# Performance work log

Measured on AMD Instinct MI355X. Metric: run time of the kernel, lower is better.

The kernel has to match this reference:

```python
import jax, jax.numpy as jnp
import numpy as np

B, V, H_DIM, W_DIM = 4, 4, 256, 384
D_SH = 1  # sh_degree=0, pred_color=False -> (0+1)^2
SCALE_MIN, SCALE_MAX = 1e-05, 30.0
EPS = 1e-08


def _quat_to_mat(q):  # (...,4) wxyz unit quat -> (...,3,3)
    w, x, y, z = q[..., 0], q[..., 1], q[..., 2], q[..., 3]
    return jnp.stack([
        jnp.stack([1 - 2 * (y * y + z * z), 2 * (x * y - w * z), 2 * (x * z + w * y)], -1),
        jnp.stack([2 * (x * y + w * z), 1 - 2 * (x * x + z * z), 2 * (y * z - w * x)], -1),
        jnp.stack([2 * (x * z - w * y), 2 * (y * z + w * x), 1 - 2 * (x * x + y * y)], -1),
    ], -2)


def _mat_to_quat_wxyz(m):  # (...,3,3) rotation -> (...,4) wxyz
    m00, m01, m02 = m[..., 0, 0], m[..., 0, 1], m[..., 0, 2]
    m10, m11, m12 = m[..., 1, 0], m[..., 1, 1], m[..., 1, 2]
    m20, m21, m22 = m[..., 2, 0], m[..., 2, 1], m[..., 2, 2]
    q_abs = jnp.sqrt(jnp.maximum(0.0, jnp.stack([
        1.0 + m00 + m11 + m22, 1.0 + m00 - m11 - m22,
        1.0 - m00 + m11 - m22, 1.0 - m00 - m11 + m22], -1)))
    cand = jnp.stack([
        jnp.stack([q_abs[..., 0] ** 2, m21 - m12, m02 - m20, m10 - m01], -1),
        jnp.stack([m21 - m12, q_abs[..., 1] ** 2, m10 + m01, m02 + m20], -1),
        jnp.stack([m02 - m20, m10 + m01, q_abs[..., 2] ** 2, m12 + m21], -1),
        jnp.stack([m10 - m01, m20 + m02, m21 + m12, q_abs[..., 3] ** 2], -1),
    ], -2)
    cand = cand / (2.0 * jnp.maximum(q_abs[..., None], 0.1))
    idx = jnp.argmax(q_abs, axis=-1)
    q = jnp.take_along_axis(cand, idx[..., None, None], axis=-2)[..., 0, :]
    return q / jnp.linalg.norm(q, axis=-1, keepdims=True)


def _quat_mul_wxyz(a, b):
    aw, ax, ay, az = a[..., 0], a[..., 1], a[..., 2], a[..., 3]
    bw, bx, by, bz = b[..., 0], b[..., 1], b[..., 2], b[..., 3]
    return jnp.stack([
        aw * bw - ax * bx - ay * by - az * bz,
        aw * bx + ax * bw + ay * bz - az * by,
        aw * by - ax * bz + ay * bw + az * bx,
        aw * bz + ax * by - ay * bx + az * bw], -1)


def setup_inputs() -> dict:
    key = jax.random.key(0)
    k1, k2, k3, k4, k5, k6 = jax.random.split(key, 6)
    # valid world->cam extrinsics: rotation from random unit quats + translation
    q = jax.random.normal(k1, (B, V, 4), jnp.float32)
    q = q / jnp.linalg.norm(q, axis=-1, keepdims=True)
    R = _quat_to_mat(q)
    t = jax.random.normal(k2, (B, V, 3), jnp.float32)
    ext = jnp.zeros((B, V, 4, 4), jnp.float32)
    ext = ext.at[..., :3, :3].set(R).at[..., :3, 3].set(t).at[..., 3, 3].set(1.0)
    # pixel-unit intrinsics
    f = W_DIM * (0.8 + 0.4 * jax.random.uniform(k3, (B, V), jnp.float32))
    intr = jnp.zeros((B, V, 3, 3), jnp.float32)
    intr = (intr.at[..., 0, 0].set(f).at[..., 1, 1].set(f)
                .at[..., 0, 2].set(W_DIM / 2).at[..., 1, 2].set(H_DIM / 2)
                .at[..., 2, 2].set(1.0))
    depths = 0.5 + 9.5 * jax.random.uniform(k4, (B, V, H_DIM, W_DIM), jnp.float32)
    opac = jax.random.uniform(k5, (B, V, H_DIM, W_DIM), jnp.float32)
    raw = jax.random.normal(k6, (B, V, H_DIM, W_DIM, 12), jnp.float32)
    return {"extrinsics": ext, "intrinsics": intr, "depths": depths,
            "opacities": opac, "raw_gaussians": raw, "H": H_DIM, "W": W_DIM}


def reference(extrinsics, intrinsics, depths, opacities, raw_gaussians, H, W):
    raw = raw_gaussians
    b, v = raw.shape[:2]
    dtype = raw.dtype
    # cam2world = affine inverse of world2cam extrinsics
    Rw2c = extrinsics[..., :3, :3]
    t = extrinsics[..., :3, 3]
    Rc2w = jnp.swapaxes(Rw2c, -1, -2)                       # (b,v,3,3)
    origins = -jnp.einsum('bvij,bvj->bvi', Rc2w, t)          # (b,v,3) camera centers
    # normalized intrinsics (detached in the original)
    intr_n = jax.lax.stop_gradient(intrinsics) * jnp.array(
        [[1.0 / W], [1.0 / H], [1.0]], dtype=intrinsics.dtype)
    # pixel-center grid in normalized [0,1] coords, (x, y) order
    xs = (jnp.arange(W, dtype=dtype) + 0.5) / W
    ys = (jnp.arange(H, dtype=dtype) + 0.5) / H
    xy = jnp.stack(jnp.meshgrid(xs, ys, indexing='xy'), -1)  # (H,W,2)
    pixel_size = jnp.array([1.0 / W, 1.0 / H], dtype=dtype)
    xy = xy[None, None] + raw[..., :2] * pixel_size          # (b,v,H,W,2) with xy offset
    # unproject: K^-1 @ [x,y,1], normalize, rotate into world
    Kinv = jnp.linalg.inv(intr_n)                            # (b,v,3,3)
    homog = jnp.concatenate([xy, jnp.ones_like(xy[..., :1])], -1)
    d_cam = jnp.einsum('bvij,bvhwj->bvhwi', Kinv, homog)
    d_cam = d_cam / jnp.linalg.norm(d_cam, axis=-1, keepdims=True)
    d_world = jnp.einsum('bvij,bvhwj->bvhwi', Rc2w, d_cam)
    means = origins[:, :, None, None] + d_world * depths[..., None]
    means = means.reshape(b, -1, 3)
    # scales: sigmoid squash then metric scaling by depth * intrinsics multiplier
    scales = SCALE_MIN + (SCALE_MAX - SCALE_MIN) * jax.nn.sigmoid(raw[..., 2:5])
    k2 = intr_n[..., :2, :2]
    det = k2[..., 0, 0] * k2[..., 1, 1] - k2[..., 0, 1] * k2[..., 1, 0]
    inv2 = jnp.stack([
        jnp.stack([k2[..., 1, 1], -k2[..., 0, 1]], -1),
        jnp.stack([-k2[..., 1, 0], k2[..., 0, 0]], -1)], -2) / det[..., None, None]
    mult = 0.1 * jnp.einsum('bvij,j->bvi', inv2, pixel_size).sum(-1)  # (b,v)
    gs_scales = (scales * depths[..., None] * mult[:, :, None, None, None]).reshape(b, -1, 3)
    # rotations: normalize predicted cam quat (xyzw), compose with c2w rotation -> world wxyz
    rot = raw[..., 5:9]
    rot = rot / (jnp.linalg.norm(rot, axis=-1, keepdims=True) + EPS)
    cam_q_wxyz = jnp.concatenate([rot[..., 3:4], rot[..., :3]], -1)
    c2w_q = _mat_to_quat_wxyz(Rc2w)                          # (b,v,4)
    world_q = _quat_mul_wxyz(c2w_q[:, :, None, None, :], cam_q_wxyz)
    rotations = world_q.reshape(b, -1, 4)
    # spherical harmonics: degree 0 -> sh_mask is all ones, no SH rotation
    harmonics = raw[..., 9:12].reshape(b, -1, 3, D_SH)
    opac = opacities.reshape(b, -1)
    return means, gs_scales, rotations, harmonics, opac
```

## Files before the change

### kernel.cpp

```cpp
#include <hip/hip_runtime.h>
#include <math.h>

#define Bc 4
#define Vc 4
#define Hc 256
#define Wc 384
#define HWc (Hc*Wc)
#define TOTc (Bc*Vc*HWc)
#define SCALE_MIN_c 1e-05f
#define SCALE_MAX_c 30.0f
#define EPS_c 1e-08f

#define MEANS_OFF  ((size_t)0)
#define SCALES_OFF ((size_t)TOTc*3)
#define ROT_OFF    ((size_t)TOTc*6)
#define HARM_OFF   ((size_t)TOTc*10)
#define OPAC_OFF   ((size_t)TOTc*13)

__global__ __launch_bounds__(256, 4) void ga_kernel(
    const float* __restrict__ ext,
    const float* __restrict__ intr,
    const float* __restrict__ depths,
    const float* __restrict__ opac,
    const float* __restrict__ raw,
    float* __restrict__ out)
{
    __shared__ float sM[4][768];
    __shared__ float sS[4][768];
    __shared__ float sH[4][768];

    const int tid  = threadIdx.x;
    const int lane = tid & 63;
    const int wv   = tid >> 6;
    const int waveBase = blockIdx.x * 1024 + wv * 256;
    const int bview    = blockIdx.x / 96;
    const int pvBase   = (blockIdx.x - bview * 96) * 1024 + wv * 256;
    float* sMw = sM[wv];
    float* sSw = sS[wv];
    float* sHw = sH[wv];

    const float4* r4 = reinterpret_cast<const float4*>(raw) + (size_t)waveBase * 3;
    const int li = 3 * lane;
    const float4 v0 = r4[      li+0], v1 = r4[      li+1], v2 = r4[      li+2];
    const float  d0 = depths[waveBase       + lane];
    const float  p0 = opac  [waveBase       + lane];
    const float4 v3 = r4[192 + li+0], v4 = r4[192 + li+1], v5 = r4[192 + li+2];
    const float  d1 = depths[waveBase +  64 + lane];
    const float  p1 = opac  [waveBase +  64 + lane];
    const float4 v6 = r4[384 + li+0], v7 = r4[384 + li+1], v8 = r4[384 + li+2];
    const float  d2 = depths[waveBase + 128 + lane];
    const float  p2 = opac  [waveBase + 128 + lane];
    const float4 v9 = r4[576 + li+0], v10= r4[576 + li+1], v11= r4[576 + li+2];
    const float  d3 = depths[waveBase + 192 + lane];
    const float  p3 = opac  [waveBase + 192 + lane];

    const float* E = ext  + bview * 16;
    const float* I = intr + bview * 9;

    const float R0 = E[0], R1 = E[4], R2 = E[8];
    const float R3 = E[1], R4 = E[5], R5 = E[9];
    const float R6 = E[2], R7 = E[6], R8 = E[10];
    const float t0 = E[3], t1 = E[7], t2 = E[11];
    const float O0 = -(R0*t0 + R1*t1 + R2*t2);
    const float O1 = -(R3*t0 + R4*t1 + R5*t2);
    const float O2 = -(R6*t0 + R7*t1 + R8*t2);

    const float a00 = I[0]*(1.0f/Wc), a01 = I[1]*(1.0f/Wc), a02 = I[2]*(1.0f/Wc);
    const float a10 = I[3]*(1.0f/Hc), a11 = I[4]*(1.0f/Hc), a12 = I[5]*(1.0f/Hc);
    const float a20 = I[6],           a21 = I[7],           a22 = I[8];
    const float det = a00*(a11*a22 - a12*a21)
                    - a01*(a10*a22 - a12*a20)
                    + a02*(a10*a21 - a11*a20);
    const float id = 1.0f / det;
    const float K0 = (a11*a22 - a12*a21)*id;
    const float K1 = (a02*a21 - a01*a22)*id;
    const float K2 = (a01*a12 - a02*a11)*id;
    const float K3 = (a12*a20 - a10*a22)*id;
    const float K4 = (a00*a22 - a02*a20)*id;
    const float K5 = (a02*a10 - a00*a12)*id;
    const float K6 = (a10*a21 - a11*a20)*id;
    const float K7 = (a01*a20 - a00*a21)*id;
    const float K8 = (a00*a11 - a01*a10)*id;

    const float det2 = a00*a11 - a01*a10;
    const float mult = 0.1f * ((a11*(1.0f/Wc) - a01*(1.0f/Hc))
                             + (-a10*(1.0f/Wc) + a00*(1.0f/Hc))) / det2;

    const float qa0 = sqrtf(fmaxf(0.0f, 1.0f + R0 + R4 + R8));
    const float qa1 = sqrtf(fmaxf(0.0f, 1.0f + R0 - R4 - R8));
    const float qa2 = sqrtf(fmaxf(0.0f, 1.0f - R0 + R4 - R8));
    const float qa3 = sqrtf(fmaxf(0.0f, 1.0f - R0 - R4 + R8));
    float bq = qa0;
    float b0 = qa0*qa0, b1 = R7 - R5, b2 = R2 - R6, b3 = R3 - R1;
    {
        const bool s1 = qa1 > bq;
        b0 = s1 ? (R7 - R5)   : b0;
        b1 = s1 ? (qa1*qa1)   : b1;
        b2 = s1 ? (R3 + R1)   : b2;
        b3 = s1 ? (R2 + R6)   : b3;
        bq = s1 ? qa1 : bq;
        const bool s2 = qa2 > bq;
        b0 = s2 ? (R2 - R6)   : b0;
        b1 = s2 ? (R3 + R1)   : b1;
        b2 = s2 ? (qa2*qa2)   : b2;
        b3 = s2 ? (R5 + R7)   : b3;
        bq = s2 ? qa2 : bq;
        const bool s3 = qa3 > bq;
        b0 = s3 ? (R3 - R1)   : b0;
        b1 = s3 ? (R6 + R2)   : b1;
        b2 = s3 ? (R7 + R5)   : b2;
        b3 = s3 ? (qa3*qa3)   : b3;
        bq = s3 ? qa3 : bq;
    }
    const float dd = 1.0f / (2.0f * fmaxf(bq, 0.1f));
    const float q0 = b0*dd, q1 = b1*dd, q2 = b2*dd, q3 = b3*dd;
    const float qn = 1.0f / sqrtf(q0*q0 + q1*q1 + q2*q2 + q3*q3);
    const float aw = q0*qn, ax = q1*qn, ay = q2*qn, az = q3*qn;

    auto PIX = [&](const float4 A, const float4 Bq, const float4 C,
                   const float dep, const int p, const int sbase) -> float4 {
        const int h = p / Wc;
        const int w = p - h * Wc;
        const float x = (w + 0.5f) * (1.0f/Wc) + A.x * (1.0f/Wc);
        const float y = (h + 0.5f) * (1.0f/Hc) + A.y * (1.0f/Hc);

        float dc0 = K0*x + K1*y + K2;
        float dc1 = K3*x + K4*y + K5;
        float dc2 = K6*x + K7*y + K8;
        const float inl = rsqrtf(dc0*dc0 + dc1*dc1 + dc2*dc2);
        dc0 *= inl; dc1 *= inl; dc2 *= inl;

        const float dw0 = R0*dc0 + R1*dc1 + R2*dc2;
        const float dw1 = R3*dc0 + R4*dc1 + R5*dc2;
        const float dw2 = R6*dc0 + R7*dc1 + R8*dc2;

        sMw[sbase+0] = O0 + dw0*dep;
        sMw[sbase+1] = O1 + dw1*dep;
        sMw[sbase+2] = O2 + dw2*dep;

        const float sm = dep * mult;
        sSw[sbase+0] = (SCALE_MIN_c + (SCALE_MAX_c - SCALE_MIN_c) / (1.0f + __expf(-A.z))) * sm;
        sSw[sbase+1] = (SCALE_MIN_c + (SCALE_MAX_c - SCALE_MIN_c) / (1.0f + __expf(-A.w))) * sm;
        sSw[sbase+2] = (SCALE_MIN_c + (SCALE_MAX_c - SCALE_MIN_c) / (1.0f + __expf(-Bq.x))) * sm;

        sHw[sbase+0] = C.y;
        sHw[sbase+1] = C.z;
        sHw[sbase+2] = C.w;

        const float rx = Bq.y, ry = Bq.z, rz = Bq.w, rw = C.x;
        const float rn = 1.0f / (sqrtf(rx*rx + ry*ry + rz*rz + rw*rw) + EPS_c);
        const float bwq = rw*rn, bxq = rx*rn, byq = ry*rn, bzq = rz*rn;
        float4 wq;
        wq.x = aw*bwq - ax*bxq - ay*byq - az*bzq;
        wq.y = aw*bxq + ax*bwq + ay*bzq - az*byq;
        wq.z = aw*byq - ax*bzq + ay*bwq + az*bxq;
        wq.w = aw*bzq + ax*byq - ay*bxq + az*bwq;
        return wq;
    };

    float4* outR4 = reinterpret_cast<float4*>(out + ROT_OFF);

    outR4[waveBase       + lane] = PIX(v0, v1, v2,  d0, pvBase       + lane, (      lane)*3);
    out[OPAC_OFF + waveBase       + lane] = p0;
    outR4[waveBase +  64 + lane] = PIX(v3, v4, v5,  d1, pvBase +  64 + lane, ( 64 + lane)*3);
    out[OPAC_OFF + waveBase +  64 + lane] = p1;
    outR4[waveBase + 128 + lane] = PIX(v6, v7, v8,  d2, pvBase + 128 + lane, (128 + lane)*3);
    out[OPAC_OFF + waveBase + 128 + lane] = p2;
    outR4[waveBase + 192 + lane] = PIX(v9, v10,v11, d3, pvBase + 192 + lane, (192 + lane)*3);
    out[OPAC_OFF + waveBase + 192 + lane] = p3;

    __syncthreads();

    {
        const float4* sv = reinterpret_cast<const float4*>(sMw);
        float4* o = reinterpret_cast<float4*>(out + MEANS_OFF + (size_t)waveBase * 3);
        o[lane] = sv[lane];  o[64 + lane] = sv[64 + lane];  o[128 + lane] = sv[128 + lane];
    }
    {
        const float4* sv = reinterpret_cast<const float4*>(sSw);
        float4* o = reinterpret_cast<float4*>(out + SCALES_OFF + (size_t)waveBase * 3);
        o[lane] = sv[lane];  o[64 + lane] = sv[64 + lane];  o[128 + lane] = sv[128 + lane];
    }
    {
        const float4* sv = reinterpret_cast<const float4*>(sHw);
        float4* o = reinterpret_cast<float4*>(out + HARM_OFF + (size_t)waveBase * 3);
        o[lane] = sv[lane];  o[64 + lane] = sv[64 + lane];  o[128 + lane] = sv[128 + lane];
    }
}

extern "C" void kernel_launch(void* const* d_in, const int* in_sizes, int n_in,
                              void* d_out, int out_size, void* d_ws, size_t ws_size,
                              hipStream_t stream) {
    const float* ext    = (const float*)d_in[0];
    const float* intr   = (const float*)d_in[1];
    const float* depths = (const float*)d_in[2];
    const float* opac   = (const float*)d_in[3];
    const float* raw    = (const float*)d_in[4];
    float* out = (float*)d_out;

    ga_kernel<<<TOTc / 1024, 256, 0, stream>>>(ext, intr, depths, opac, raw, out);
}
```

Measured before the change: 171.7 us.

## Process two tiles per block, prefetching both tiles' inputs before compute

Each block now handles two 1024-pixel tiles, with all loads for both tiles issued up front so more memory requests are in flight per wave. Per-view camera setup is amortized over twice the pixels, and the grid is halved. This costs roughly double the register footprint for the held inputs (launch bounds lowered to 3), and adds extra barriers so the shared staging buffers can be reused between the two tiles.

```diff
diff --git a/kernel.cpp b/kernel.cpp
--- a/kernel.cpp
+++ b/kernel.cpp
@@ -17,7 +17,7 @@
 #define HARM_OFF   ((size_t)TOTc*10)
 #define OPAC_OFF   ((size_t)TOTc*13)
 
-__global__ __launch_bounds__(256, 4) void ga_kernel(
+__global__ __launch_bounds__(256, 3) void ga_kernel(
     const float* __restrict__ ext,
     const float* __restrict__ intr,
     const float* __restrict__ depths,
@@ -32,27 +32,45 @@
     const int tid  = threadIdx.x;
     const int lane = tid & 63;
     const int wv   = tid >> 6;
-    const int waveBase = blockIdx.x * 1024 + wv * 256;
-    const int bview    = blockIdx.x / 96;
-    const int pvBase   = (blockIdx.x - bview * 96) * 1024 + wv * 256;
+    const int tA   = blockIdx.x * 2;
+    const int bview = tA / 96;
+    const int waveBaseA = tA * 1024 + wv * 256;
+    const int waveBaseB = waveBaseA + 1024;
+    const int pvBaseA   = (tA - bview * 96) * 1024 + wv * 256;
+    const int pvBaseB   = pvBaseA + 1024;
     float* sMw = sM[wv];
     float* sSw = sS[wv];
     float* sHw = sH[wv];
 
-    const float4* r4 = reinterpret_cast<const float4*>(raw) + (size_t)waveBase * 3;
     const int li = 3 * lane;
-    const float4 v0 = r4[      li+0], v1 = r4[      li+1], v2 = r4[      li+2];
-    const float  d0 = depths[waveBase       + lane];
-    const float  p0 = opac  [waveBase       + lane];
-    const float4 v3 = r4[192 + li+0], v4 = r4[192 + li+1], v5 = r4[192 + li+2];
-    const float  d1 = depths[waveBase +  64 + lane];
-    const float  p1 = opac  [waveBase +  64 + lane];
-    const float4 v6 = r4[384 + li+0], v7 = r4[384 + li+1], v8 = r4[384 + li+2];
-    const float  d2 = depths[waveBase + 128 + lane];
-    const float  p2 = opac  [waveBase + 128 + lane];
-    const float4 v9 = r4[576 + li+0], v10= r4[576 + li+1], v11= r4[576 + li+2];
-    const float  d3 = depths[waveBase + 192 + lane];
-    const float  p3 = opac  [waveBase + 192 + lane];
+
+    const float4* r4A = reinterpret_cast<const float4*>(raw) + (size_t)waveBaseA * 3;
+    const float4* r4B = reinterpret_cast<const float4*>(raw) + (size_t)waveBaseB * 3;
+
+    float4 va[12], vb[12];
+    float  da[4], pa[4], db[4], pb[4];
+    #pragma unroll
+    for (int k = 0; k < 4; ++k) {
+        va[3*k+0] = r4A[192*k + li + 0];
+        va[3*k+1] = r4A[192*k + li + 1];
+        va[3*k+2] = r4A[192*k + li + 2];
+    }
+    #pragma unroll
+    for (int k = 0; k < 4; ++k) {
+        da[k] = depths[waveBaseA + 64*k + lane];
+        pa[k] = opac  [waveBaseA + 64*k + lane];
+    }
+    #pragma unroll
+    for (int k = 0; k < 4; ++k) {
+        vb[3*k+0] = r4B[192*k + li + 0];
+        vb[3*k+1] = r4B[192*k + li + 1];
+        vb[3*k+2] = r4B[192*k + li + 2];
+    }
+    #pragma unroll
+    for (int k = 0; k < 4; ++k) {
+        db[k] = depths[waveBaseB + 64*k + lane];
+        pb[k] = opac  [waveBaseB + 64*k + lane];
+    }
 
     const float* E = ext  + bview * 16;
     const float* I = intr + bview * 9;
@@ -160,31 +178,56 @@
 
     float4* outR4 = reinterpret_cast<float4*>(out + ROT_OFF);
 
-    outR4[waveBase       + lane] = PIX(v0, v1, v2,  d0, pvBase       + lane, (      lane)*3);
-    out[OPAC_OFF + waveBase       + lane] = p0;
-    outR4[waveBase +  64 + lane] = PIX(v3, v4, v5,  d1, pvBase +  64 + lane, ( 64 + lane)*3);
-    out[OPAC_OFF + waveBase +  64 + lane] = p1;
-    outR4[waveBase + 128 + lane] = PIX(v6, v7, v8,  d2, pvBase + 128 + lane, (128 + lane)*3);
-    out[OPAC_OFF + waveBase + 128 + lane] = p2;
-    outR4[waveBase + 192 + lane] = PIX(v9, v10,v11, d3, pvBase + 192 + lane, (192 + lane)*3);
-    out[OPAC_OFF + waveBase + 192 + lane] = p3;
+    #pragma unroll
+    for (int k = 0; k < 4; ++k) {
+        outR4[waveBaseA + 64*k + lane] =
+            PIX(va[3*k], va[3*k+1], va[3*k+2], da[k],
+                pvBaseA + 64*k + lane, (64*k + lane)*3);
+        out[OPAC_OFF + waveBaseA + 64*k + lane] = pa[k];
+    }
 
     __syncthreads();
 
     {
-        const float4* sv = reinterpret_cast<const float4*>(sMw);
-        float4* o = reinterpret_cast<float4*>(out + MEANS_OFF + (size_t)waveBase * 3);
-        o[lane] = sv[lane];  o[64 + lane] = sv[64 + lane];  o[128 + lane] = sv[128 + lane];
-    }
+        const float4* svM = reinterpret_cast<const float4*>(sMw);
+        const float4* svS = reinterpret_cast<const float4*>(sSw);
+        const float4* svH = reinterpret_cast<const float4*>(sHw);
+        float4* oM = reinterpret_cast<float4*>(out + MEANS_OFF  + (size_t)waveBaseA * 3);
+        float4* oS = reinterpret_cast<float4*>(out + SCALES_OFF + (size_t)waveBaseA * 3);
+        float4* oH = reinterpret_cast<float4*>(out + HARM_OFF   + (size_t)waveBaseA * 3);
+        #pragma unroll
+        for (int k = 0; k < 3; ++k) {
+            oM[64*k + lane] = svM[64*k + lane];
+            oS[64*k + lane] = svS[64*k + lane];
+            oH[64*k + lane] = svH[64*k + lane];
+        }
+    }
+
+    __syncthreads();
+
+    #pragma unroll
+    for (int k = 0; k < 4; ++k) {
+        outR4[waveBaseB + 64*k + lane] =
+            PIX(vb[3*k], vb[3*k+1], vb[3*k+2], db[k],
+                pvBaseB + 64*k + lane, (64*k + lane)*3);
+        out[OPAC_OFF + waveBaseB + 64*k + lane] = pb[k];
+    }
+
+    __syncthreads();
+
     {
-        const float4* sv = reinterpret_cast<const float4*>(sSw);
-        float4* o = reinterpret_cast<float4*>(out + SCALES_OFF + (size_t)waveBase * 3);
-        o[lane] = sv[lane];  o[64 + lane] = sv[64 + lane];  o[128 + lane] = sv[128 + lane];
-    }
-    {
-        const float4* sv = reinterpret_cast<const float4*>(sHw);
-        float4* o = reinterpret_cast<float4*>(out + HARM_OFF + (size_t)waveBase * 3);
-        o[lane] = sv[lane];  o[64 + lane] = sv[64 + lane];  o[128 + lane] = sv[128 + lane];
+        const float4* svM = reinterpret_cast<const float4*>(sMw);
+        const float4* svS = reinterpret_cast<const float4*>(sSw);
+        const float4* svH = reinterpret_cast<const float4*>(sHw);
+        float4* oM = reinterpret_cast<float4*>(out + MEANS_OFF  + (size_t)waveBaseB * 3);
+        float4* oS = reinterpret_cast<float4*>(out + SCALES_OFF + (size_t)waveBaseB * 3);
+        float4* oH = reinterpret_cast<float4*>(out + HARM_OFF   + (size_t)waveBaseB * 3);
+        #pragma unroll
+        for (int k = 0; k < 3; ++k) {
+            oM[64*k + lane] = svM[64*k + lane];
+            oS[64*k + lane] = svS[64*k + lane];
+            oH[64*k + lane] = svH[64*k + lane];
+        }
     }
 }
 
@@ -198,5 +241,5 @@
     const float* raw    = (const float*)d_in[4];
     float* out = (float*)d_out;
 
-    ga_kernel<<<TOTc / 1024, 256, 0, stream>>>(ext, intr, depths, opac, raw, out);
+    ga_kernel<<<TOTc / 2048, 256, 0, stream>>>(ext, intr, depths, opac, raw, out);
 }
```

Result: no change. 174.5 us (+1.6%).
